# Performance work log

Measured on AMD Instinct MI355X. Metric: run time of the kernel, lower is better.

Reference implementation:

```python
import jax, jax.numpy as jnp
import numpy as np

B, N, H = 16, 8192, 128
TOK_MLP, CH_MLP = 256, 512
EPS = 1e-5


def _layer_norm(z, g, b):
    m = jnp.mean(z, axis=-1, keepdims=True)
    v = jnp.mean(jnp.square(z - m), axis=-1, keepdims=True)
    return (z - m) * jax.lax.rsqrt(v + EPS) * g + b


def setup_inputs() -> dict:
    key = jax.random.key(0)
    ks = jax.random.split(key, 9)
    s = 0.02
    return {
        "x": jax.random.normal(ks[0], (B, N, H), dtype=jnp.float32),
        "ln1_g": jnp.ones((H,), jnp.float32),
        "ln1_b": jnp.zeros((H,), jnp.float32),
        "ln2_g": jnp.ones((H,), jnp.float32),
        "ln2_b": jnp.zeros((H,), jnp.float32),
        "tok_w1": jax.random.normal(ks[1], (N, TOK_MLP), jnp.float32) * s,
        "tok_b1": jnp.zeros((TOK_MLP,), jnp.float32),
        "tok_w2": jax.random.normal(ks[2], (TOK_MLP, N), jnp.float32) * s,
        "tok_b2": jnp.zeros((N,), jnp.float32),
        "ch_w1": jax.random.normal(ks[3], (H, CH_MLP), jnp.float32) * s,
        "ch_b1": jnp.zeros((CH_MLP,), jnp.float32),
        "ch_w2": jax.random.normal(ks[4], (CH_MLP, H), jnp.float32) * s,
        "ch_b2": jnp.zeros((H,), jnp.float32),
    }


def reference(x, ln1_g, ln1_b, ln2_g, ln2_b,
              tok_w1, tok_b1, tok_w2, tok_b2,
              ch_w1, ch_b1, ch_w2, ch_b2):
    # x: [B, N, H]
    y = _layer_norm(x, ln1_g, ln1_b)
    # mask-expand-multiply-sum over dim=2 == reverse (suffix) cumsum over tokens:
    # out[b, j, h] = sum_{i >= j} y[b, i, h]
    y = jnp.flip(jnp.cumsum(jnp.flip(y, axis=1), axis=1), axis=1)  # [B, N, H]
    y = jnp.swapaxes(y, 1, 2)                                      # [B, H, N]
    h = jax.nn.gelu(y @ tok_w1 + tok_b1, approximate=False)        # [B, H, TOK_MLP]
    y = h @ tok_w2 + tok_b2                                        # [B, H, N]
    y = jnp.swapaxes(y, 1, 2)                                      # [B, N, H]
    y = _layer_norm(y, ln2_g, ln2_b)
    h = jax.nn.gelu(y @ ch_w1 + ch_b1, approximate=False)          # [B, N, CH_MLP]
    return h @ ch_w2 + ch_b2                                       # [B, N, H]
```

## Files before the change

kernel.cpp:

```cpp
#include <hip/hip_runtime.h>
#include <math.h>

#define B_ 16
#define N_ 8192
#define H_ 128
#define T_ 256
#define C_ 512

typedef __bf16 bf16x8 __attribute__((ext_vector_type(8)));
typedef __bf16 bf16x4 __attribute__((ext_vector_type(4)));
typedef float f32x4 __attribute__((ext_vector_type(4)));

__device__ __forceinline__ float gelu_f(float x) {
    float p = fmaf(0.044715f * x * x, x, x);
    float e = __expf(-1.5957691216057308f * p);
    return x * __builtin_amdgcn_rcpf(1.f + e);
}

__device__ __forceinline__ unsigned short f2bf(float x) {
    unsigned int u = __float_as_uint(x);
    u = (u + 0x7FFFu + ((u >> 16) & 1u)) >> 16;
    return (unsigned short)u;
}

__device__ __forceinline__ void gl2lds16(const void* g, void* l) {
    __builtin_amdgcn_global_load_lds(
        (const __attribute__((address_space(1))) void*)g,
        (__attribute__((address_space(3))) void*)l,
        16, 0, 0);
}

__global__ void k_w1_psum(const float* __restrict__ w1, float* __restrict__ psum) {
    int c = blockIdx.x, t = threadIdx.x;
    const float* p = w1 + (size_t)c * 64 * T_ + t;
    float s = 0.f;
    #pragma unroll 8
    for (int r = 0; r < 64; ++r) s += p[(size_t)r * T_];
    psum[c * T_ + t] = s;
}

__global__ void k_w1_scan(const float* __restrict__ psum, float* __restrict__ offs) {
    int t = threadIdx.x;
    float run = 0.f;
    for (int c = 0; c < 128; ++c) {
        offs[c * T_ + t] = run;
        run += psum[c * T_ + t];
    }
}

__global__ void k_w1_prefix(const float* __restrict__ w1, const float* __restrict__ offs,
                            unsigned short* __restrict__ w1ct) {
    int c = blockIdx.x, t = threadIdx.x;
    float run = offs[c * T_ + t];
    const float* p = w1 + (size_t)c * 64 * T_ + t;
    unsigned int wb[32];
    #pragma unroll
    for (int q = 0; q < 32; ++q) {
        run += p[(size_t)(2 * q) * T_];
        unsigned int lo = f2bf(run);
        run += p[(size_t)(2 * q + 1) * T_];
        wb[q] = lo | ((unsigned int)f2bf(run) << 16);
    }
    char* row = (char*)w1ct + ((size_t)t * N_ + c * 64) * 2;
    int key = (t & 7) << 4;
    #pragma unroll
    for (int pc = 0; pc < 8; ++pc) {
        int4 v = { (int)wb[4*pc], (int)wb[4*pc+1], (int)wb[4*pc+2], (int)wb[4*pc+3] };
        *(int4*)(row + ((pc * 16) ^ key)) = v;
    }
}

__global__ void k_w2t_pack(const float* __restrict__ w2, unsigned short* __restrict__ w2t) {
    __shared__ float ld[64 * 68];
    int nt = blockIdx.x, tt = blockIdx.y;
    int n0 = nt * 64, t0 = tt * 64;
    int tid = threadIdx.x;
    #pragma unroll
    for (int rnd = 0; rnd < 4; ++rnd) {
        int idx = tid + rnd * 256;
        int tr = idx >> 4, nc = idx & 15;
        float4 v = *(const float4*)(w2 + (size_t)(t0 + tr) * N_ + n0 + nc * 4);
        *(float4*)&ld[tr * 68 + nc * 4] = v;
    }
    __syncthreads();
    int n = tid >> 2, q = tid & 3;
    int key = (n & 7) << 4;
    unsigned int wb[8];
    #pragma unroll
    for (int j = 0; j < 8; ++j) {
        float a = ld[(q * 16 + 2 * j) * 68 + n];
        float b = ld[(q * 16 + 2 * j + 1) * 68 + n];
        wb[j] = (unsigned int)f2bf(a) | ((unsigned int)f2bf(b) << 16);
    }
    char* row = (char*)w2t + (size_t)(n0 + n) * 512 + t0 * 2;
    int4 v0 = { (int)wb[0], (int)wb[1], (int)wb[2], (int)wb[3] };
    int4 v1 = { (int)wb[4], (int)wb[5], (int)wb[6], (int)wb[7] };
    *(int4*)(row + ((q * 32) ^ key)) = v0;
    *(int4*)(row + ((q * 32 + 16) ^ key)) = v1;
}

__global__ void k_pack1(const float* __restrict__ w1, unsigned short* __restrict__ w1p) {
    int e = blockIdx.x * 256 + threadIdx.x;
    int c = e >> 13, t = e & 8191;
    int n = t >> 7, j = t & 127;
    int k = j ^ ((n & 7) << 3);
    int hid = c * 64 + n;
    w1p[e] = f2bf(w1[(size_t)k * C_ + hid]);
}

__global__ void k_pack2(const float* __restrict__ w2, unsigned short* __restrict__ w2p) {
    int e = blockIdx.x * 256 + threadIdx.x;
    int c = e >> 13, t = e & 8191;
    int n = t >> 6, j = t & 63;
    int k = j ^ ((n & 7) << 3);
    w2p[e] = f2bf(w2[(size_t)(c * 64 + k) * H_ + n]);
}

__global__ void k_lnT(const float* __restrict__ x, const float* __restrict__ g,
                      const float* __restrict__ bb, unsigned short* __restrict__ y1t) {
    __shared__ float ln[64 * 129];
    int tid = threadIdx.x;
    int wave = tid >> 6, lane = tid & 63;
    size_t base = (size_t)blockIdx.x * 64;
    float2 gg = *(const float2*)(g + lane * 2);
    float2 bv = *(const float2*)(bb + lane * 2);
    for (int rr = 0; rr < 16; ++rr) {
        int r = wave * 16 + rr;
        float2 v = *(const float2*)(x + (base + r) * H_ + lane * 2);
        float s = v.x + v.y, ss = v.x * v.x + v.y * v.y;
        #pragma unroll
        for (int off = 32; off; off >>= 1) { s += __shfl_xor(s, off); ss += __shfl_xor(ss, off); }
        float mean = s * (1.f / 128.f);
        float rstd = rsqrtf(ss * (1.f / 128.f) - mean * mean + 1e-5f);
        ln[r * 129 + lane * 2]     = (v.x - mean) * rstd * gg.x + bv.x;
        ln[r * 129 + lane * 2 + 1] = (v.y - mean) * rstd * gg.y + bv.y;
    }
    __syncthreads();
    int h = tid >> 1, half = tid & 1;
    unsigned int wb[16];
    #pragma unroll
    for (int q = 0; q < 16; ++q) {
        float a = ln[(half * 32 + 2 * q) * 129 + h];
        float b = ln[(half * 32 + 2 * q + 1) * 129 + h];
        wb[q] = (unsigned int)f2bf(a) | ((unsigned int)f2bf(b) << 16);
    }
    int b_ = (int)(base >> 13);
    int n0 = (int)(base & (N_ - 1));
    char* row = (char*)y1t + (((size_t)b_ * H_ + h) * N_ + n0) * 2;
    int key = (h & 7) << 4;
    #pragma unroll
    for (int pc = 0; pc < 4; ++pc) {
        int4 v = { (int)wb[4*pc], (int)wb[4*pc+1], (int)wb[4*pc+2], (int)wb[4*pc+3] };
        *(int4*)(row + ((half * 64 + pc * 16) ^ key)) = v;
    }
}

#define T1_YS 0
#define T1_WS 16384

__global__ __launch_bounds__(512, 1)
void k_tok1(const unsigned short* __restrict__ y1t, const unsigned short* __restrict__ w1ct,
            float* __restrict__ P) {
    __shared__ __align__(16) char sm[49152];
    int kk = blockIdx.x, b = blockIdx.y;
    int tid = threadIdx.x;
    int w = tid >> 6, lane = tid & 63;
    int lr = lane & 15, lk = lane >> 4;
    int mg = w >> 2, ng = w & 3;
    const char* yb = (const char*)y1t + (size_t)b * H_ * N_ * 2;
    const char* wbg = (const char*)w1ct;
    int kbase = kk * 512;

    f32x4 acc[4][4];
    #pragma unroll
    for (int i = 0; i < 4; ++i)
        #pragma unroll
        for (int j = 0; j < 4; ++j) acc[i][j] = (f32x4){0.f, 0.f, 0.f, 0.f};

    for (int s = 0; s < 8; ++s) {
        int n0 = kbase + s * 64;
        __syncthreads();
        #pragma unroll
        for (int rnd = 0; rnd < 2; ++rnd) {
            int idx = tid + rnd * 512;
            int hr = idx >> 3, p = idx & 7;
            gl2lds16(yb + ((size_t)hr * N_ + n0) * 2 + p * 16, sm + T1_YS + idx * 16);
        }
        #pragma unroll
        for (int rnd = 0; rnd < 4; ++rnd) {
            int idx = tid + rnd * 512;
            int tr = idx >> 3, p = idx & 7;
            gl2lds16(wbg + ((size_t)tr * N_ + n0) * 2 + p * 16, sm + T1_WS + idx * 16);
        }
        __syncthreads();
        #pragma unroll
        for (int ks = 0; ks < 2; ++ks) {
            bf16x8 af[4], bfr[4];
            #pragma unroll
            for (int i = 0; i < 4; ++i) {
                int h = mg * 64 + i * 16 + lr;
                af[i] = *(const bf16x8*)(sm + T1_YS + h * 128 + ((ks * 64 + lk * 16) ^ ((h & 7) << 4)));
            }
            #pragma unroll
            for (int j = 0; j < 4; ++j) {
                int t = ng * 64 + j * 16 + lr;
                bfr[j] = *(const bf16x8*)(sm + T1_WS + t * 128 + ((ks * 64 + lk * 16) ^ ((t & 7) << 4)));
            }
            #pragma unroll
            for (int i = 0; i < 4; ++i)
                #pragma unroll
                for (int j = 0; j < 4; ++j)
                    acc[i][j] = __builtin_amdgcn_mfma_f32_16x16x32_bf16(af[i], bfr[j], acc[i][j], 0, 0, 0);
        }
    }

    float* Pb = P + ((size_t)(b * 16 + kk)) * (H_ * T_);
    #pragma unroll
    for (int i = 0; i < 4; ++i)
        #pragma unroll
        for (int j = 0; j < 4; ++j) {
            int t = ng * 64 + j * 16 + lr;
            #pragma unroll
            for (int r = 0; r < 4; ++r) {
                int h = mg * 64 + i * 16 + lk * 4 + r;
                Pb[h * T_ + t] = acc[i][j][r];
            }
        }
}

__global__ void k_tok1_fin(const float* __restrict__ P, const float* __restrict__ b1,
                           unsigned short* __restrict__ g1b) {
    int fid = blockIdx.x * 256 + threadIdx.x;
    int base = fid * 4;
    int b = base >> 15, rem = base & 32767;
    int h = rem >> 8, t = rem & 255;
    const float* Pb = P + (size_t)b * 16 * 32768 + rem;
    float4 a = *(const float4*)Pb;
    #pragma unroll
    for (int kk = 1; kk < 16; ++kk) {
        float4 p = *(const float4*)(Pb + (size_t)kk * 32768);
        a.x += p.x; a.y += p.y; a.z += p.z; a.w += p.w;
    }
    float4 bb = *(const float4*)(b1 + t);
    unsigned int lo = (unsigned int)f2bf(gelu_f(a.x + bb.x)) | ((unsigned int)f2bf(gelu_f(a.y + bb.y)) << 16);
    unsigned int hi = (unsigned int)f2bf(gelu_f(a.z + bb.z)) | ((unsigned int)f2bf(gelu_f(a.w + bb.w)) << 16);
    char* row = (char*)g1b + (size_t)(b * H_ + h) * 512;
    uint2 v = { lo, hi };
    *(uint2*)(row + ((t * 2) ^ ((h & 7) << 4))) = v;
}

#define F_AS 0
#define F_BS 16384
#define F_YS 0
#define F_HS 0
#define F_W2 16384
#define F_W1 32768

__global__ __launch_bounds__(512, 4)
void k_tok2mlp(const unsigned short* __restrict__ g1b, const unsigned short* __restrict__ w2t,
               const float* __restrict__ tb2, const float* __restrict__ lg,
               const float* __restrict__ lb, const unsigned short* __restrict__ w1p,
               const unsigned short* __restrict__ w2p, const float* __restrict__ b1g,
               const float* __restrict__ b2g, float* __restrict__ out) {
    __shared__ __align__(16) char sm[49152];
    int nt = blockIdx.x, b = blockIdx.y;
    int tid = threadIdx.x;
    int w = tid >> 6, lane = tid & 63;
    int lr = lane & 15, lk = lane >> 4;
    const char* ab = (const char*)w2t + (size_t)(nt * 128) * 512;
    const char* gb = (const char*)g1b + (size_t)b * H_ * 512;
    const char* w1b = (const char*)w1p;
    const char* w2b = (const char*)w2p;

    f32x4 acc[8];
    #pragma unroll
    for (int g = 0; g < 8; ++g) acc[g] = (f32x4){0.f, 0.f, 0.f, 0.f};

    int arow = w * 16 + lr;
    int akey = (arow & 7) << 4;
    for (int q = 0; q < 4; ++q) {
        __syncthreads();
        #pragma unroll
        for (int rnd = 0; rnd < 2; ++rnd) {
            int idx = tid + rnd * 512;
            int row = idx >> 3, p = idx & 7;
            gl2lds16(ab + (size_t)row * 512 + q * 128 + p * 16, sm + F_AS + row * 128 + p * 16);
            gl2lds16(gb + (size_t)row * 512 + q * 128 + p * 16, sm + F_BS + row * 128 + p * 16);
        }
        __syncthreads();
        #pragma unroll
        for (int ks = 0; ks < 2; ++ks) {
            bf16x8 af = *(const bf16x8*)(sm + F_AS + arow * 128 + ((ks * 64 + lk * 16) ^ akey));
            #pragma unroll
            for (int g = 0; g < 8; ++g) {
                int hrow = g * 16 + lr;
                bf16x8 bf_ = *(const bf16x8*)(sm + F_BS + hrow * 128 + ((ks * 64 + lk * 16) ^ ((hrow & 7) << 4)));
                acc[g] = __builtin_amdgcn_mfma_f32_16x16x32_bf16(af, bf_, acc[g], 0, 0, 0);
            }
        }
    }

    float gam[8], bet[8];
    #pragma unroll
    for (int g = 0; g < 8; ++g) { gam[g] = lg[g * 16 + lr]; bet[g] = lb[g * 16 + lr]; }
    __syncthreads();

    #pragma unroll
    for (int j = 0; j < 2; ++j)
        gl2lds16(w1b + w * 2048 + j * 1024 + lane * 16, sm + F_W1 + w * 2048 + j * 1024);

    #pragma unroll
    for (int r = 0; r < 4; ++r) {
        int row = w * 16 + lk * 4 + r;
        float bias2 = tb2[nt * 128 + row];
        float vals[8];
        float s = 0.f, ss = 0.f;
        #pragma unroll
        for (int g = 0; g < 8; ++g) {
            float v = acc[g][r] + bias2;
            vals[g] = v; s += v; ss += v * v;
        }
        #pragma unroll
        for (int off = 8; off; off >>= 1) { s += __shfl_xor(s, off); ss += __shfl_xor(ss, off); }
        float mean = s * (1.f / 128.f);
        float rstd = rsqrtf(ss * (1.f / 128.f) - mean * mean + 1e-5f);
        int key = (row & 7) << 4;
        char* orow = sm + F_YS + row * 256;
        #pragma unroll
        for (int g = 0; g < 8; ++g) {
            float v = (vals[g] - mean) * rstd * gam[g] + bet[g];
            *(unsigned short*)(orow + (((g * 16 + lr) * 2) ^ key)) = f2bf(v);
        }
    }
    __syncthreads();

    int mg = w >> 1, ng = w & 1;
    int key = (lr & 7) << 4;

    bf16x8 yfrag[2][4];
    #pragma unroll
    for (int m = 0; m < 2; ++m) {
        int yrow = (2 * mg + m) * 16 + lr;
        #pragma unroll
        for (int kc = 0; kc < 4; ++kc)
            yfrag[m][kc] = *(const bf16x8*)(sm + F_YS + yrow * 256 + ((kc * 64 + lk * 16) ^ key));
    }
    __syncthreads();

    #pragma unroll
    for (int j = 0; j < 2; ++j)
        gl2lds16(w2b + w * 2048 + j * 1024 + lane * 16, sm + F_W2 + w * 2048 + j * 1024);

    f32x4 oacc[2][4];
    #pragma unroll
    for (int m = 0; m < 2; ++m)
        #pragma unroll
        for (int n = 0; n < 4; ++n) oacc[m][n] = (f32x4){0.f, 0.f, 0.f, 0.f};

    for (int c = 0; c < 8; ++c) {
        f32x4 hacc[2][2];
        #pragma unroll
        for (int n = 0; n < 2; ++n) {
            float4 bv4 = *(const float4*)(b1g + c * 64 + (2 * ng + n) * 16 + lk * 4);
            f32x4 iv = { bv4.x, bv4.y, bv4.z, bv4.w };
            hacc[0][n] = iv;
            hacc[1][n] = iv;
        }
        #pragma unroll
        for (int kc = 0; kc < 4; ++kc) {
            int ko = kc * 64 + lk * 16;
            bf16x8 b0 = *(const bf16x8*)(sm + F_W1 + ((2 * ng) * 16 + lr) * 256 + (ko ^ key));
            bf16x8 b1 = *(const bf16x8*)(sm + F_W1 + ((2 * ng + 1) * 16 + lr) * 256 + (ko ^ key));
            hacc[0][0] = __builtin_amdgcn_mfma_f32_16x16x32_bf16(b0, yfrag[0][kc], hacc[0][0], 0, 0, 0);
            hacc[0][1] = __builtin_amdgcn_mfma_f32_16x16x32_bf16(b1, yfrag[0][kc], hacc[0][1], 0, 0, 0);
            hacc[1][0] = __builtin_amdgcn_mfma_f32_16x16x32_bf16(b0, yfrag[1][kc], hacc[1][0], 0, 0, 0);
            hacc[1][1] = __builtin_amdgcn_mfma_f32_16x16x32_bf16(b1, yfrag[1][kc], hacc[1][1], 0, 0, 0);
        }
        #pragma unroll
        for (int m = 0; m < 2; ++m)
            #pragma unroll
            for (int n = 0; n < 2; ++n) {
                int tok = (2 * mg + m) * 16 + lr;
                int hid0 = (2 * ng + n) * 16 + lk * 4;
                bf16x4 pv;
                pv[0] = (__bf16)gelu_f(hacc[m][n][0]);
                pv[1] = (__bf16)gelu_f(hacc[m][n][1]);
                pv[2] = (__bf16)gelu_f(hacc[m][n][2]);
                pv[3] = (__bf16)gelu_f(hacc[m][n][3]);
                *(bf16x4*)(sm + F_HS + tok * 128 + ((hid0 * 2) ^ ((tok & 7) << 4))) = pv;
            }
        __syncthreads();
        if (c < 7) {
            #pragma unroll
            for (int j = 0; j < 2; ++j)
                gl2lds16(w1b + (c + 1) * 16384 + w * 2048 + j * 1024 + lane * 16,
                         sm + F_W1 + w * 2048 + j * 1024);
        }
        #pragma unroll
        for (int kc = 0; kc < 2; ++kc) {
            int ko = kc * 64 + lk * 16;
            int t0 = (2 * mg) * 16 + lr, t1 = (2 * mg + 1) * 16 + lr;
            bf16x8 a0 = *(const bf16x8*)(sm + F_HS + t0 * 128 + (ko ^ ((t0 & 7) << 4)));
            bf16x8 a1 = *(const bf16x8*)(sm + F_HS + t1 * 128 + (ko ^ ((t1 & 7) << 4)));
            #pragma unroll
            for (int n = 0; n < 4; ++n) {
                bf16x8 bb = *(const bf16x8*)(sm + F_W2 + ((ng * 4 + n) * 16 + lr) * 128 + (ko ^ key));
                oacc[0][n] = __builtin_amdgcn_mfma_f32_16x16x32_bf16(a0, bb, oacc[0][n], 0, 0, 0);
                oacc[1][n] = __builtin_amdgcn_mfma_f32_16x16x32_bf16(a1, bb, oacc[1][n], 0, 0, 0);
            }
        }
        __syncthreads();
        if (c < 7) {
            #pragma unroll
            for (int j = 0; j < 2; ++j)
                gl2lds16(w2b + (c + 1) * 16384 + w * 2048 + j * 1024 + lane * 16,
                         sm + F_W2 + w * 2048 + j * 1024);
        }
    }

    size_t rbase = (size_t)(b * 64 + nt) * 128;
    #pragma unroll
    for (int n = 0; n < 4; ++n) {
        int ch = (ng * 4 + n) * 16 + lr;
        float bv = b2g[ch];
        #pragma unroll
        for (int m = 0; m < 2; ++m)
            #pragma unroll
            for (int r = 0; r < 4; ++r) {
                size_t row = rbase + (2 * mg + m) * 16 + lk * 4 + r;
                out[row * H_ + ch] = oacc[m][n][r] + bv;
            }
    }
}

extern "C" void kernel_launch(void* const* d_in, const int* in_sizes, int n_in,
                              void* d_out, int out_size, void* d_ws, size_t ws_size,
                              hipStream_t stream) {
    const float* x      = (const float*)d_in[0];
    const float* ln1_g  = (const float*)d_in[1];
    const float* ln1_b  = (const float*)d_in[2];
    const float* ln2_g  = (const float*)d_in[3];
    const float* ln2_b  = (const float*)d_in[4];
    const float* tok_w1 = (const float*)d_in[5];
    const float* tok_b1 = (const float*)d_in[6];
    const float* tok_w2 = (const float*)d_in[7];
    const float* tok_b2 = (const float*)d_in[8];
    const float* ch_w1  = (const float*)d_in[9];
    const float* ch_b1  = (const float*)d_in[10];
    const float* ch_w2  = (const float*)d_in[11];
    const float* ch_b2  = (const float*)d_in[12];
    float* out = (float*)d_out;
    float* ws  = (float*)d_ws;

    float* psum = ws;
    float* offs = ws + 32768;
    unsigned short* w1ct = (unsigned short*)(ws + 65536);
    unsigned short* w2t  = (unsigned short*)(ws + 1114112);
    unsigned short* w1p  = (unsigned short*)(ws + 2162688);
    unsigned short* w2p  = (unsigned short*)(ws + 2195456);
    unsigned short* y1t  = (unsigned short*)(ws + 2228224);
    unsigned short* g1b  = (unsigned short*)(ws + 10616832);
    float* P             = ws + 10878976;

    k_w1_psum<<<dim3(128), dim3(256), 0, stream>>>(tok_w1, psum);
    k_w1_scan<<<dim3(1), dim3(256), 0, stream>>>(psum, offs);
    k_w1_prefix<<<dim3(128), dim3(256), 0, stream>>>(tok_w1, offs, w1ct);
    k_w2t_pack<<<dim3(128, 4), dim3(256), 0, stream>>>(tok_w2, w2t);
    k_pack1<<<dim3(256), dim3(256), 0, stream>>>(ch_w1, w1p);
    k_pack2<<<dim3(256), dim3(256), 0, stream>>>(ch_w2, w2p);
    k_lnT<<<dim3((B_ * N_) / 64), dim3(256), 0, stream>>>(x, ln1_g, ln1_b, y1t);
    k_tok1<<<dim3(16, 16), dim3(512), 0, stream>>>(y1t, w1ct, P);
    k_tok1_fin<<<dim3(512), dim3(256), 0, stream>>>(P, tok_b1, g1b);
    k_tok2mlp<<<dim3(64, 16), dim3(512), 0, stream>>>(g1b, w2t, tok_b2, ln2_g, ln2_b,
                                                      w1p, w2p, ch_b1, ch_b2, out);
}
```

Measured before the change: 138.6 us.

## Double-buffer LDS loads in tok1 and tok2mlp, add setprio, merge weight packs

Double-buffers global-to-LDS tile loads in k_tok1 (now 1024 threads, 96KB LDS) and in the first GEMM phase of k_tok2mlp, so the next tile loads while the current one is computed. It also wraps the MFMA loops in s_setprio, issues the w2 weight prefetch earlier, and merges the two channel-weight pack kernels into one launch. The cost is more LDS per block, which may lower occupancy of k_tok2mlp.

New measurement: 132.9 us. 4.1% less time.

```diff
diff --git a/kernel.cpp b/kernel.cpp
--- a/kernel.cpp
+++ b/kernel.cpp
@@ -99,21 +99,21 @@
     *(int4*)(row + ((q * 32 + 16) ^ key)) = v1;
 }
 
-__global__ void k_pack1(const float* __restrict__ w1, unsigned short* __restrict__ w1p) {
+__global__ void k_packw(const float* __restrict__ w1, const float* __restrict__ w2,
+                        unsigned short* __restrict__ w1p, unsigned short* __restrict__ w2p) {
     int e = blockIdx.x * 256 + threadIdx.x;
-    int c = e >> 13, t = e & 8191;
-    int n = t >> 7, j = t & 127;
-    int k = j ^ ((n & 7) << 3);
-    int hid = c * 64 + n;
-    w1p[e] = f2bf(w1[(size_t)k * C_ + hid]);
-}
-
-__global__ void k_pack2(const float* __restrict__ w2, unsigned short* __restrict__ w2p) {
-    int e = blockIdx.x * 256 + threadIdx.x;
-    int c = e >> 13, t = e & 8191;
-    int n = t >> 6, j = t & 63;
-    int k = j ^ ((n & 7) << 3);
-    w2p[e] = f2bf(w2[(size_t)(c * 64 + k) * H_ + n]);
+    if (blockIdx.y == 0) {
+        int c = e >> 13, t = e & 8191;
+        int n = t >> 7, j = t & 127;
+        int k = j ^ ((n & 7) << 3);
+        int hid = c * 64 + n;
+        w1p[e] = f2bf(w1[(size_t)k * C_ + hid]);
+    } else {
+        int c = e >> 13, t = e & 8191;
+        int n = t >> 6, j = t & 63;
+        int k = j ^ ((n & 7) << 3);
+        w2p[e] = f2bf(w2[(size_t)(c * 64 + k) * H_ + n]);
+    }
 }
 
 __global__ void k_lnT(const float* __restrict__ x, const float* __restrict__ g,
@@ -155,13 +155,12 @@
     }
 }
 
-#define T1_YS 0
-#define T1_WS 16384
-
-__global__ __launch_bounds__(512, 1)
+#define T1_BUF 49152
+
+__global__ __launch_bounds__(1024, 2)
 void k_tok1(const unsigned short* __restrict__ y1t, const unsigned short* __restrict__ w1ct,
             float* __restrict__ P) {
-    __shared__ __align__(16) char sm[49152];
+    __shared__ __align__(16) char sm[98304];
     int kk = blockIdx.x, b = blockIdx.y;
     int tid = threadIdx.x;
     int w = tid >> 6, lane = tid & 63;
@@ -171,58 +170,69 @@
     const char* wbg = (const char*)w1ct;
     int kbase = kk * 512;
 
-    f32x4 acc[4][4];
-    #pragma unroll
-    for (int i = 0; i < 4; ++i)
+    f32x4 acc[2][4];
+    #pragma unroll
+    for (int i = 0; i < 2; ++i)
         #pragma unroll
         for (int j = 0; j < 4; ++j) acc[i][j] = (f32x4){0.f, 0.f, 0.f, 0.f};
 
+    {
+        int hr = tid >> 3, p = tid & 7;
+        gl2lds16(yb + ((size_t)hr * N_ + kbase) * 2 + p * 16, sm + tid * 16);
+        #pragma unroll
+        for (int rnd = 0; rnd < 2; ++rnd) {
+            int idx = tid + rnd * 1024;
+            int tr = idx >> 3, pp = idx & 7;
+            gl2lds16(wbg + ((size_t)tr * N_ + kbase) * 2 + pp * 16, sm + 16384 + idx * 16);
+        }
+    }
+    __syncthreads();
+
     for (int s = 0; s < 8; ++s) {
-        int n0 = kbase + s * 64;
-        __syncthreads();
-        #pragma unroll
-        for (int rnd = 0; rnd < 2; ++rnd) {
-            int idx = tid + rnd * 512;
-            int hr = idx >> 3, p = idx & 7;
-            gl2lds16(yb + ((size_t)hr * N_ + n0) * 2 + p * 16, sm + T1_YS + idx * 16);
-        }
-        #pragma unroll
-        for (int rnd = 0; rnd < 4; ++rnd) {
-            int idx = tid + rnd * 512;
-            int tr = idx >> 3, p = idx & 7;
-            gl2lds16(wbg + ((size_t)tr * N_ + n0) * 2 + p * 16, sm + T1_WS + idx * 16);
-        }
-        __syncthreads();
+        const char* cur = sm + (s & 1) * T1_BUF;
+        if (s < 7) {
+            char* nxt = sm + ((s + 1) & 1) * T1_BUF;
+            int n0 = kbase + (s + 1) * 64;
+            int hr = tid >> 3, p = tid & 7;
+            gl2lds16(yb + ((size_t)hr * N_ + n0) * 2 + p * 16, nxt + tid * 16);
+            #pragma unroll
+            for (int rnd = 0; rnd < 2; ++rnd) {
+                int idx = tid + rnd * 1024;
+                int tr = idx >> 3, pp = idx & 7;
+                gl2lds16(wbg + ((size_t)tr * N_ + n0) * 2 + pp * 16, nxt + 16384 + idx * 16);
+            }
+        }
         #pragma unroll
         for (int ks = 0; ks < 2; ++ks) {
-            bf16x8 af[4], bfr[4];
-            #pragma unroll
-            for (int i = 0; i < 4; ++i) {
-                int h = mg * 64 + i * 16 + lr;
-                af[i] = *(const bf16x8*)(sm + T1_YS + h * 128 + ((ks * 64 + lk * 16) ^ ((h & 7) << 4)));
+            bf16x8 af[2], bfr[4];
+            #pragma unroll
+            for (int i = 0; i < 2; ++i) {
+                int h = mg * 32 + i * 16 + lr;
+                af[i] = *(const bf16x8*)(cur + h * 128 + ((ks * 64 + lk * 16) ^ ((h & 7) << 4)));
             }
             #pragma unroll
             for (int j = 0; j < 4; ++j) {
                 int t = ng * 64 + j * 16 + lr;
-                bfr[j] = *(const bf16x8*)(sm + T1_WS + t * 128 + ((ks * 64 + lk * 16) ^ ((t & 7) << 4)));
-            }
-            #pragma unroll
-            for (int i = 0; i < 4; ++i)
+                bfr[j] = *(const bf16x8*)(cur + 16384 + t * 128 + ((ks * 64 + lk * 16) ^ ((t & 7) << 4)));
+            }
+            #pragma unroll
+            for (int i = 0; i < 2; ++i)
                 #pragma unroll
                 for (int j = 0; j < 4; ++j)
                     acc[i][j] = __builtin_amdgcn_mfma_f32_16x16x32_bf16(af[i], bfr[j], acc[i][j], 0, 0, 0);
         }
+        __syncthreads();
     }
 
     float* Pb = P + ((size_t)(b * 16 + kk)) * (H_ * T_);
     #pragma unroll
-    for (int i = 0; i < 4; ++i)
+    for (int i = 0; i < 2; ++i)
         #pragma unroll
         for (int j = 0; j < 4; ++j) {
             int t = ng * 64 + j * 16 + lr;
             #pragma unroll
             for (int r = 0; r < 4; ++r) {
-                int h = mg * 64 + i * 16 + lk * 4 + r;
+                int h = mg * 32 + i * 16 + lk * 4 + r;
                 Pb[h * T_ + t] = acc[i][j][r];
             }
         }
@@ -249,12 +259,10 @@
     *(uint2*)(row + ((t * 2) ^ ((h & 7) << 4))) = v;
 }
 
-#define F_AS 0
-#define F_BS 16384
 #define F_YS 0
 #define F_HS 0
-#define F_W2 16384
-#define F_W1 32768
+#define F_W2 32768
+#define F_W1 49152
 
 __global__ __launch_bounds__(512, 4)
 void k_tok2mlp(const unsigned short* __restrict__ g1b, const unsigned short* __restrict__ w2t,
@@ -262,7 +270,7 @@
                const float* __restrict__ lb, const unsigned short* __restrict__ w1p,
                const unsigned short* __restrict__ w2p, const float* __restrict__ b1g,
                const float* __restrict__ b2g, float* __restrict__ out) {
-    __shared__ __align__(16) char sm[49152];
+    __shared__ __align__(16) char sm[65536];
     int nt = blockIdx.x, b = blockIdx.y;
     int tid = threadIdx.x;
     int w = tid >> 6, lane = tid & 63;
@@ -278,36 +286,52 @@
 
     int arow = w * 16 + lr;
     int akey = (arow & 7) << 4;
+
+    #pragma unroll
+    for (int rnd = 0; rnd < 2; ++rnd) {
+        int idx = tid + rnd * 512;
+        int row = idx >> 3, p = idx & 7;
+        gl2lds16(ab + (size_t)row * 512 + p * 16, sm + row * 128 + p * 16);
+        gl2lds16(gb + (size_t)row * 512 + p * 16, sm + 16384 + row * 128 + p * 16);
+    }
+    __syncthreads();
+
     for (int q = 0; q < 4; ++q) {
-        __syncthreads();
-        #pragma unroll
-        for (int rnd = 0; rnd < 2; ++rnd) {
-            int idx = tid + rnd * 512;
-            int row = idx >> 3, p = idx & 7;
-            gl2lds16(ab + (size_t)row * 512 + q * 128 + p * 16, sm + F_AS + row * 128 + p * 16);
-            gl2lds16(gb + (size_t)row * 512 + q * 128 + p * 16, sm + F_BS + row * 128 + p * 16);
-        }
-        __syncthreads();
+        const char* cur = sm + (q & 1) * 32768;
+        if (q < 3) {
+            char* nxt = sm + ((q + 1) & 1) * 32768;
+            #pragma unroll
+            for (int rnd = 0; rnd < 2; ++rnd) {
+                int idx = tid + rnd * 512;
+                int row = idx >> 3, p = idx & 7;
+                gl2lds16(ab + (size_t)row * 512 + (q + 1) * 128 + p * 16, nxt + row * 128 + p * 16);
+                gl2lds16(gb + (size_t)row * 512 + (q + 1) * 128 + p * 16, nxt + 16384 + row * 128 + p * 16);
+            }
+        }
+        __builtin_amdgcn_s_setprio(1);
         #pragma unroll
         for (int ks = 0; ks < 2; ++ks) {
-            bf16x8 af = *(const bf16x8*)(sm + F_AS + arow * 128 + ((ks * 64 + lk * 16) ^ akey));
+            bf16x8 af = *(const bf16x8*)(cur + arow * 128 + ((ks * 64 + lk * 16) ^ akey));
             #pragma unroll
             for (int g = 0; g < 8; ++g) {
                 int hrow = g * 16 + lr;
-                bf16x8 bf_ = *(const bf16x8*)(sm + F_BS + hrow * 128 + ((ks * 64 + lk * 16) ^ ((hrow & 7) << 4)));
+                bf16x8 bf_ = *(const bf16x8*)(cur + 16384 + hrow * 128 + ((ks * 64 + lk * 16) ^ ((hrow & 7) << 4)));
                 acc[g] = __builtin_amdgcn_mfma_f32_16x16x32_bf16(af, bf_, acc[g], 0, 0, 0);
             }
         }
+        __builtin_amdgcn_s_setprio(0);
+        __syncthreads();
     }
 
     float gam[8], bet[8];
     #pragma unroll
     for (int g = 0; g < 8; ++g) { gam[g] = lg[g * 16 + lr]; bet[g] = lb[g * 16 + lr]; }
-    __syncthreads();
-
-    #pragma unroll
-    for (int j = 0; j < 2; ++j)
+
+    #pragma unroll
+    for (int j = 0; j < 2; ++j) {
         gl2lds16(w1b + w * 2048 + j * 1024 + lane * 16, sm + F_W1 + w * 2048 + j * 1024);
+        gl2lds16(w2b + w * 2048 + j * 1024 + lane * 16, sm + F_W2 + w * 2048 + j * 1024);
+    }
 
     #pragma unroll
     for (int r = 0; r < 4; ++r) {
@@ -347,10 +371,6 @@
     }
     __syncthreads();
 
-    #pragma unroll
-    for (int j = 0; j < 2; ++j)
-        gl2lds16(w2b + w * 2048 + j * 1024 + lane * 16, sm + F_W2 + w * 2048 + j * 1024);
-
     f32x4 oacc[2][4];
     #pragma unroll
     for (int m = 0; m < 2; ++m)
@@ -366,6 +386,7 @@
             hacc[0][n] = iv;
             hacc[1][n] = iv;
         }
+        __builtin_amdgcn_s_setprio(1);
         #pragma unroll
         for (int kc = 0; kc < 4; ++kc) {
             int ko = kc * 64 + lk * 16;
@@ -376,6 +397,7 @@
             hacc[1][0] = __builtin_amdgcn_mfma_f32_16x16x32_bf16(b0, yfrag[1][kc], hacc[1][0], 0, 0, 0);
             hacc[1][1] = __builtin_amdgcn_mfma_f32_16x16x32_bf16(b1, yfrag[1][kc], hacc[1][1], 0, 0, 0);
         }
+        __builtin_amdgcn_s_setprio(0);
         #pragma unroll
         for (int m = 0; m < 2; ++m)
             #pragma unroll
@@ -396,6 +418,7 @@
                 gl2lds16(w1b + (c + 1) * 16384 + w * 2048 + j * 1024 + lane * 16,
                          sm + F_W1 + w * 2048 + j * 1024);
         }
+        __builtin_amdgcn_s_setprio(1);
         #pragma unroll
         for (int kc = 0; kc < 2; ++kc) {
             int ko = kc * 64 + lk * 16;
@@ -409,6 +432,7 @@
                 oacc[1][n] = __builtin_amdgcn_mfma_f32_16x16x32_bf16(a1, bb, oacc[1][n], 0, 0, 0);
             }
         }
+        __builtin_amdgcn_s_setprio(0);
         __syncthreads();
         if (c < 7) {
             #pragma unroll
@@ -466,10 +490,9 @@
     k_w1_scan<<<dim3(1), dim3(256), 0, stream>>>(psum, offs);
     k_w1_prefix<<<dim3(128), dim3(256), 0, stream>>>(tok_w1, offs, w1ct);
     k_w2t_pack<<<dim3(128, 4), dim3(256), 0, stream>>>(tok_w2, w2t);
-    k_pack1<<<dim3(256), dim3(256), 0, stream>>>(ch_w1, w1p);
-    k_pack2<<<dim3(256), dim3(256), 0, stream>>>(ch_w2, w2p);
+    k_packw<<<dim3(256, 2), dim3(256), 0, stream>>>(ch_w1, ch_w2, w1p, w2p);
     k_lnT<<<dim3((B_ * N_) / 64), dim3(256), 0, stream>>>(x, ln1_g, ln1_b, y1t);
-    k_tok1<<<dim3(16, 16), dim3(512), 0, stream>>>(y1t, w1ct, P);
+    k_tok1<<<dim3(16, 16), dim3(1024), 0, stream>>>(y1t, w1ct, P);
     k_tok1_fin<<<dim3(512), dim3(256), 0, stream>>>(P, tok_b1, g1b);
     k_tok2mlp<<<dim3(64, 16), dim3(512), 0, stream>>>(g1b, w2t, tok_b2, ln2_g, ln2_b,
                                                       w1p, w2p, ch_b1, ch_b2, out);
```
